# Kernel optimization log

Measured on AMD Instinct MI355X. Metric: run time of the kernel, lower is better.

## Reference

```python
import jax, jax.numpy as jnp
import numpy as np

N, E = 8192, 65536
IN_C, OUT_C, EF = 64, 16, 8
L1, L2 = 48, 32  # in - floor((in-out)/3), in - floor(2*(in-out)/3)


def setup_inputs() -> dict:
    key = jax.random.key(0)
    ks = jax.random.split(key, 10)
    rn = lambda k, shape, s: jax.random.normal(k, shape, dtype=jnp.float32) * s
    return {
        "x": jax.random.normal(ks[0], (N, IN_C), dtype=jnp.float32),
        "edge_index": jax.random.randint(ks[1], (2, E), 0, N, dtype=jnp.int32),
        "edge_attr": jax.random.normal(ks[2], (E, EF), dtype=jnp.float32),
        "nn1_w": rn(ks[3], (EF, IN_C * L1), 0.05),
        "nn1_b": jnp.zeros((IN_C * L1,), jnp.float32),
        "root1": rn(ks[4], (IN_C, L1), 0.1),
        "bias1": jnp.zeros((L1,), jnp.float32),
        "nn2_w": rn(ks[5], (EF, L1 * L2), 0.05),
        "nn2_b": jnp.zeros((L1 * L2,), jnp.float32),
        "root2": rn(ks[6], (L1, L2), 0.1),
        "bias2": jnp.zeros((L2,), jnp.float32),
        "mu_w": rn(ks[7], (L2, OUT_C), 0.1),
        "mu_b": jnp.zeros((OUT_C,), jnp.float32),
        "ls_w": rn(ks[8], (L2, OUT_C), 0.1),
        "ls_b": jnp.zeros((OUT_C,), jnp.float32),
    }


def _nnconv(x, src, dst, edge_attr, nn_w, nn_b, root, bias, c_in, c_out):
    # edge MLP -> per-edge weight matrices [E, c_in, c_out]
    w = (edge_attr @ nn_w + nn_b).reshape(-1, c_in, c_out)
    msg = jnp.einsum('ei,eio->eo', x[src], w)  # gather + per-edge matvec
    agg = jax.ops.segment_sum(msg, dst, num_segments=x.shape[0])  # sum aggregation
    return agg + x @ root + bias  # root transform + bias


def _gcn(x, src, dst, w, b):
    n = x.shape[0]
    # degree over target nodes, including self-loop (edge_weight = 1)
    deg = jax.ops.segment_sum(jnp.ones_like(src, jnp.float32), dst, num_segments=n) + 1.0
    dinv = jax.lax.rsqrt(deg)
    h = x @ w
    norm = dinv[src] * dinv[dst]  # [E]
    agg = jax.ops.segment_sum(h[src] * norm[:, None], dst, num_segments=n)
    return agg + h * (1.0 / deg)[:, None] + b  # self-loop contribution: deg_i^{-1}


def reference(x, edge_index, edge_attr, nn1_w, nn1_b, root1, bias1,
              nn2_w, nn2_b, root2, bias2, mu_w, mu_b, ls_w, ls_b):
    src, dst = edge_index[0], edge_index[1]
    h = jax.nn.relu(_nnconv(x, src, dst, edge_attr, nn1_w, nn1_b, root1, bias1, IN_C, L1))
    h = jax.nn.relu(_nnconv(h, src, dst, edge_attr, nn2_w, nn2_b, root2, bias2, L1, L2))
    return (_gcn(h, src, dst, mu_w, mu_b), _gcn(h, src, dst, ls_w, ls_b))
```

## Files before the change

kernel.cpp:

```cpp
#include <hip/hip_runtime.h>

#define NN 8192
#define EE 65536
#define MAXDEG 32
#define ZS1 652
#define ZS2 492
#define U1_OFF 5216
#define U2_OFF 3936


__global__ __launch_bounds__(256) void k_zero(int* __restrict__ cnt,
                                              int* __restrict__ ssrcb,
                                              float* __restrict__ seab) {
    int n = blockIdx.x * 256 + threadIdx.x;
    cnt[n] = 0;
    ssrcb[n * MAXDEG] = 0;
    float4* p = (float4*)(seab + (size_t)n * MAXDEG * 8);
    p[0] = make_float4(0.f, 0.f, 0.f, 0.f);
    p[1] = make_float4(0.f, 0.f, 0.f, 0.f);
}

__global__ __launch_bounds__(256) void k_bucket(const int* __restrict__ ei,
                                                const float* __restrict__ ea,
                                                int* __restrict__ cnt,
                                                int* __restrict__ ssrcb,
                                                float* __restrict__ seab) {
    int e = blockIdx.x * 256 + threadIdx.x;
    if (e >= EE) return;
    int s = ei[e], d = ei[EE + e];
    int pos = atomicAdd(&cnt[d], 1);
    if (pos < MAXDEG) {
        int slot = d * MAXDEG + pos;
        ssrcb[slot] = s;
        const float4* a = (const float4*)(ea + (size_t)e * 8);
        float4* bp = (float4*)(seab + (size_t)slot * 8);
        bp[0] = a[0];
        bp[1] = a[1];
    }
}

__global__ __launch_bounds__(256) void k_L1(const int* __restrict__ cnt,
                                            const int* __restrict__ ssrcb,
                                            const float* __restrict__ seab,
                                            const float* __restrict__ x,
                                            const float* __restrict__ nn1_w,
                                            const float* __restrict__ nn1_b,
                                            const float* __restrict__ root1,
                                            const float* __restrict__ bias1,
                                            float* __restrict__ h1) {
    __shared__ __align__(16) float smem[U1_OFF + 3072];
    float* Zt = smem;
    float* U  = smem + U1_OFF;
    const int n0 = blockIdx.x * 8;
    {
        const int wv = threadIdx.x >> 6;
        const int i = threadIdx.x & 63;
        const int nnA = wv * 2, nnB = nnA + 1;
        const int rsA = (n0 + nnA) * MAXDEG;
        const int rsB = (n0 + nnB) * MAXDEG;
        int dA = cnt[n0 + nnA]; if (dA > MAXDEG) dA = MAXDEG;
        int dB = cnt[n0 + nnB]; if (dB > MAXDEG) dB = MAXDEG;
        const int eA = rsA + dA, eB = rsB + dB;
        int jA = rsA, jB = rsB;
        float aA[8] = {0, 0, 0, 0, 0, 0, 0, 0}, sA = 0.f;
        float aB[8] = {0, 0, 0, 0, 0, 0, 0, 0}, sB = 0.f;
        while (jA < eA || jB < eB) {
            int cjA[8], cjB[8];
#pragma unroll
            for (int p = 0; p < 8; p++) {
                int ja = jA + p; cjA[p] = (ja < eA) ? ja : rsA;
                int jb = jB + p; cjB[p] = (jb < eB) ? jb : rsB;
            }
            int sjA[8], sjB[8];
#pragma unroll
            for (int p = 0; p < 8; p++) { sjA[p] = ssrcb[cjA[p]]; sjB[p] = ssrcb[cjB[p]]; }
            float xvA[8], xvB[8];
#pragma unroll
            for (int p = 0; p < 8; p++) {
                xvA[p] = x[(size_t)sjA[p] * 64 + i];
                xvB[p] = x[(size_t)sjB[p] * 64 + i];
            }
#pragma unroll
            for (int p = 0; p < 8; p++) {
                {
                    const float4* q4 = (const float4*)(seab + (size_t)cjA[p] * 8);
                    float4 e0 = q4[0], e1 = q4[1];
                    float xx = (jA + p < eA) ? xvA[p] : 0.f;
                    aA[0] += e0.x * xx; aA[1] += e0.y * xx; aA[2] += e0.z * xx; aA[3] += e0.w * xx;
                    aA[4] += e1.x * xx; aA[5] += e1.y * xx; aA[6] += e1.z * xx; aA[7] += e1.w * xx;
                    sA += xx;
                }
                {
                    const float4* q4 = (const float4*)(seab + (size_t)cjB[p] * 8);
                    float4 e0 = q4[0], e1 = q4[1];
                    float xx = (jB + p < eB) ? xvB[p] : 0.f;
                    aB[0] += e0.x * xx; aB[1] += e0.y * xx; aB[2] += e0.z * xx; aB[3] += e0.w * xx;
                    aB[4] += e1.x * xx; aB[5] += e1.y * xx; aB[6] += e1.z * xx; aB[7] += e1.w * xx;
                    sB += xx;
                }
            }
            jA += 8; jB += 8;
        }
        float* zrA = Zt + nnA * ZS1;
        float* zrB = Zt + nnB * ZS1;
#pragma unroll
        for (int f = 0; f < 8; f++) { zrA[f * 64 + i] = aA[f]; zrB[f * 64 + i] = aB[f]; }
        zrA[512 + i] = sA; zrB[512 + i] = sB;
        zrA[576 + i] = x[(size_t)(n0 + nnA) * 64 + i];
        zrB[576 + i] = x[(size_t)(n0 + nnB) * 64 + i];
    }
    const int o  = threadIdx.x & 15;
    const int q  = (threadIdx.x >> 4) & 1;
    const int ks = threadIdx.x >> 5;
    float acc[4][3];
#pragma unroll
    for (int m = 0; m < 4; m++)
#pragma unroll
        for (int cc = 0; cc < 3; cc++) acc[m][cc] = 0.f;
    for (int c = 0; c < 10; ++c) {
        __syncthreads();
        const float* src = (c < 8) ? nn1_w + c * 3072 : (c == 8 ? nn1_b : root1);
#pragma unroll
        for (int i2 = 0; i2 < 3; i2++) {
            int g = threadIdx.x + i2 * 256;
            *(float4*)&U[g * 4] = *(const float4*)&src[g * 4];
        }
        __syncthreads();
        const int kl0 = ks * 8;
        const int kg0 = c * 64 + kl0;
#pragma unroll
        for (int kk = 0; kk < 8; kk += 4) {
            const int kl = kl0 + kk, kg = kg0 + kk;
            float zc[4][4];
#pragma unroll
            for (int m = 0; m < 4; m++) {
                float4 z = *(const float4*)&Zt[(q * 4 + m) * ZS1 + kg];
                zc[m][0] = z.x; zc[m][1] = z.y; zc[m][2] = z.z; zc[m][3] = z.w;
            }
#pragma unroll
            for (int dk = 0; dk < 4; dk++) {
                float w0 = U[(kl + dk) * 48 + o];
                float w1 = U[(kl + dk) * 48 + o + 16];
                float w2 = U[(kl + dk) * 48 + o + 32];
#pragma unroll
                for (int m = 0; m < 4; m++) {
                    acc[m][0] += zc[m][dk] * w0;
                    acc[m][1] += zc[m][dk] * w1;
                    acc[m][2] += zc[m][dk] * w2;
                }
            }
        }
    }
    __syncthreads();
#pragma unroll
    for (int m = 0; m < 4; m++) {
        U[(ks * 8 + q * 4 + m) * 48 + o]      = acc[m][0];
        U[(ks * 8 + q * 4 + m) * 48 + o + 16] = acc[m][1];
        U[(ks * 8 + q * 4 + m) * 48 + o + 32] = acc[m][2];
    }
    __syncthreads();
    for (int r = threadIdx.x; r < 8 * 48; r += 256) {
        int nn = r / 48, oc = r - nn * 48;
        float v = bias1[oc];
#pragma unroll
        for (int k = 0; k < 8; k++) v += U[(k * 8 + nn) * 48 + oc];
        h1[(size_t)(n0 + nn) * 48 + oc] = v > 0.f ? v : 0.f;
    }
}

__global__ __launch_bounds__(256) void k_L2(const int* __restrict__ cnt,
                                            const int* __restrict__ ssrcb,
                                            const float* __restrict__ seab,
                                            const float* __restrict__ h1,
                                            const float* __restrict__ nn2_w,
                                            const float* __restrict__ nn2_b,
                                            const float* __restrict__ root2,
                                            const float* __restrict__ bias2,
                                            const float* __restrict__ mu_w,
                                            const float* __restrict__ mu_b,
                                            const float* __restrict__ ls_w,
                                            const float* __restrict__ ls_b,
                                            float* __restrict__ hmu,
                                            float* __restrict__ hls,
                                            float* __restrict__ dinv,
                                            float* __restrict__ out) {
    __shared__ __align__(16) float smem[U2_OFF + 3072];
    float* Zt = smem;
    float* U  = smem + U2_OFF;
    const int n0 = blockIdx.x * 8;
    {
        const int wv = threadIdx.x >> 6;
        const int i = threadIdx.x & 63;
        if (i < 48) {
            const int nnA = wv * 2, nnB = nnA + 1;
            const int rsA = (n0 + nnA) * MAXDEG;
            const int rsB = (n0 + nnB) * MAXDEG;
            int dA = cnt[n0 + nnA]; if (dA > MAXDEG) dA = MAXDEG;
            int dB = cnt[n0 + nnB]; if (dB > MAXDEG) dB = MAXDEG;
            const int eA = rsA + dA, eB = rsB + dB;
            int jA = rsA, jB = rsB;
            float aA[8] = {0, 0, 0, 0, 0, 0, 0, 0}, sA = 0.f;
            float aB[8] = {0, 0, 0, 0, 0, 0, 0, 0}, sB = 0.f;
            while (jA < eA || jB < eB) {
                int cjA[8], cjB[8];
#pragma unroll
                for (int p = 0; p < 8; p++) {
                    int ja = jA + p; cjA[p] = (ja < eA) ? ja : rsA;
                    int jb = jB + p; cjB[p] = (jb < eB) ? jb : rsB;
                }
                int sjA[8], sjB[8];
#pragma unroll
                for (int p = 0; p < 8; p++) { sjA[p] = ssrcb[cjA[p]]; sjB[p] = ssrcb[cjB[p]]; }
                float hvA[8], hvB[8];
#pragma unroll
                for (int p = 0; p < 8; p++) {
                    hvA[p] = h1[(size_t)sjA[p] * 48 + i];
                    hvB[p] = h1[(size_t)sjB[p] * 48 + i];
                }
#pragma unroll
                for (int p = 0; p < 8; p++) {
                    {
                        const float4* q4 = (const float4*)(seab + (size_t)cjA[p] * 8);
                        float4 e0 = q4[0], e1 = q4[1];
                        float xx = (jA + p < eA) ? hvA[p] : 0.f;
                        aA[0] += e0.x * xx; aA[1] += e0.y * xx; aA[2] += e0.z * xx; aA[3] += e0.w * xx;
                        aA[4] += e1.x * xx; aA[5] += e1.y * xx; aA[6] += e1.z * xx; aA[7] += e1.w * xx;
                        sA += xx;
                    }
                    {
                        const float4* q4 = (const float4*)(seab + (size_t)cjB[p] * 8);
                        float4 e0 = q4[0], e1 = q4[1];
                        float xx = (jB + p < eB) ? hvB[p] : 0.f;
                        aB[0] += e0.x * xx; aB[1] += e0.y * xx; aB[2] += e0.z * xx; aB[3] += e0.w * xx;
                        aB[4] += e1.x * xx; aB[5] += e1.y * xx; aB[6] += e1.z * xx; aB[7] += e1.w * xx;
                        sB += xx;
                    }
                }
                jA += 8; jB += 8;
            }
            float* zrA = Zt + nnA * ZS2;
            float* zrB = Zt + nnB * ZS2;
#pragma unroll
            for (int f = 0; f < 8; f++) { zrA[f * 48 + i] = aA[f]; zrB[f * 48 + i] = aB[f]; }
            zrA[384 + i] = sA; zrB[384 + i] = sB;
            zrA[432 + i] = h1[(size_t)(n0 + nnA) * 48 + i];
            zrB[432 + i] = h1[(size_t)(n0 + nnB) * 48 + i];
        }
    }
    const int o  = threadIdx.x & 15;
    const int q  = (threadIdx.x >> 4) & 1;
    const int ks = threadIdx.x >> 5;
    float acc[4][2];
#pragma unroll
    for (int m = 0; m < 4; m++) { acc[m][0] = 0.f; acc[m][1] = 0.f; }
    for (int c = 0; c < 5; ++c) {
        __syncthreads();
#pragma unroll
        for (int i2 = 0; i2 < 3; i2++) {
            int g = threadIdx.x + i2 * 256;
            const float* s4;
            if (c < 4)        s4 = nn2_w + c * 3072 + g * 4;
            else if (g < 384) s4 = nn2_b + g * 4;
            else              s4 = root2 + (g - 384) * 4;
            *(float4*)&U[g * 4] = *(const float4*)s4;
        }
        __syncthreads();
        const int kl0 = ks * 12;
        const int kg0 = c * 96 + kl0;
#pragma unroll
        for (int kk = 0; kk < 12; kk += 4) {
            const int kl = kl0 + kk, kg = kg0 + kk;
            float zc[4][4];
#pragma unroll
            for (int m = 0; m < 4; m++) {
                float4 z = *(const float4*)&Zt[(q * 4 + m) * ZS2 + kg];
                zc[m][0] = z.x; zc[m][1] = z.y; zc[m][2] = z.z; zc[m][3] = z.w;
            }
#pragma unroll
            for (int dk = 0; dk < 4; dk++) {
                float w0 = U[(kl + dk) * 32 + o];
                float w1 = U[(kl + dk) * 32 + o + 16];
#pragma unroll
                for (int m = 0; m < 4; m++) {
                    acc[m][0] += zc[m][dk] * w0;
                    acc[m][1] += zc[m][dk] * w1;
                }
            }
        }
    }
    __syncthreads();
#pragma unroll
    for (int m = 0; m < 4; m++) {
        U[(ks * 8 + q * 4 + m) * 32 + o]      = acc[m][0];
        U[(ks * 8 + q * 4 + m) * 32 + o + 16] = acc[m][1];
    }
    __syncthreads();
    {
        int nn = threadIdx.x >> 5, oc = threadIdx.x & 31;
        float v = bias2[oc];
#pragma unroll
        for (int k = 0; k < 8; k++) v += U[(k * 8 + nn) * 32 + oc];
        U[2048 + nn * 33 + oc] = v > 0.f ? v : 0.f;
    }
    __syncthreads();
    if (threadIdx.x < 128) {
        const int oc = threadIdx.x & 15;
        const int nn = threadIdx.x >> 4;
        const int gn = n0 + nn;
        float am = 0.f, al = 0.f;
#pragma unroll
        for (int i = 0; i < 32; i++) {
            float hv = U[2048 + nn * 33 + i];
            am += hv * mu_w[i * 16 + oc];
            al += hv * ls_w[i * 16 + oc];
        }
        float d = (float)cnt[gn] + 1.0f;
        float di = rsqrtf(d);
        if (oc == 0) dinv[gn] = di;
        hmu[(size_t)gn * 16 + oc] = am;
        hls[(size_t)gn * 16 + oc] = al;
        out[(size_t)gn * 16 + oc] = am / d + mu_b[oc];
        out[(size_t)NN * 16 + (size_t)gn * 16 + oc] = al / d + ls_b[oc];
    }
}

__global__ __launch_bounds__(256) void k_gcn(const int* __restrict__ cnt,
                                             const int* __restrict__ ssrcb,
                                             const float* __restrict__ hmu,
                                             const float* __restrict__ hls,
                                             const float* __restrict__ dinv,
                                             float* __restrict__ out) {
    const int wave = threadIdx.x >> 6;
    const int lane = threadIdx.x & 63;
    const int o = lane & 15, p = lane >> 4;
    const int d = blockIdx.x * 4 + wave;
    int deg = cnt[d]; if (deg > MAXDEG) deg = MAXDEG;
    const int rs = d * MAXDEG, re = rs + deg;
    float am = 0.f, al = 0.f;
    for (int j = rs + p; j < re; j += 4) {
        int s = ssrcb[j];
        float ds_ = dinv[s];
        am += hmu[(size_t)s * 16 + o] * ds_;
        al += hls[(size_t)s * 16 + o] * ds_;
    }
    am += __shfl_xor(am, 16); al += __shfl_xor(al, 16);
    am += __shfl_xor(am, 32); al += __shfl_xor(al, 32);
    if (p == 0) {
        float dd = dinv[d];
        out[(size_t)d * 16 + o] += am * dd;
        out[(size_t)NN * 16 + (size_t)d * 16 + o] += al * dd;
    }
}

extern "C" void kernel_launch(void* const* d_in, const int* in_sizes, int n_in,
                              void* d_out, int out_size, void* d_ws, size_t ws_size,
                              hipStream_t stream) {
    const float* x     = (const float*)d_in[0];
    const int*   ei    = (const int*)d_in[1];
    const float* ea    = (const float*)d_in[2];
    const float* nn1_w = (const float*)d_in[3];
    const float* nn1_b = (const float*)d_in[4];
    const float* root1 = (const float*)d_in[5];
    const float* bias1 = (const float*)d_in[6];
    const float* nn2_w = (const float*)d_in[7];
    const float* nn2_b = (const float*)d_in[8];
    const float* root2 = (const float*)d_in[9];
    const float* bias2 = (const float*)d_in[10];
    const float* mu_w  = (const float*)d_in[11];
    const float* mu_b  = (const float*)d_in[12];
    const float* ls_w  = (const float*)d_in[13];
    const float* ls_b  = (const float*)d_in[14];
    float* out = (float*)d_out;

    float* W    = (float*)d_ws;
    float* seab = W;
    float* h1   = seab + NN * MAXDEG * 8;
    float* hmu  = h1 + 393216;
    float* hls  = hmu + 131072;
    float* dinv = hls + 131072;
    int* cnt    = (int*)(dinv + 8192);
    int* ssrcb  = cnt + 8192;

    k_zero<<<dim3(NN / 256), dim3(256), 0, stream>>>(cnt, ssrcb, seab);
    k_bucket<<<dim3(EE / 256), dim3(256), 0, stream>>>(ei, ea, cnt, ssrcb, seab);
    k_L1<<<dim3(NN / 8), dim3(256), 0, stream>>>(cnt, ssrcb, seab, x,
                                                 nn1_w, nn1_b, root1, bias1, h1);
    k_L2<<<dim3(NN / 8), dim3(256), 0, stream>>>(cnt, ssrcb, seab, h1,
                                                 nn2_w, nn2_b, root2, bias2,
                                                 mu_w, mu_b, ls_w, ls_b,
                                                 hmu, hls, dinv, out);
    k_gcn<<<dim3(NN / 4), dim3(256), 0, stream>>>(cnt, ssrcb,
                                                  hmu, hls, dinv, out);
}
```

Measured before the change: 149.5 us.

## Pre-transpose edge-MLP weights, swizzle LDS tiles, prefetch weight chunks, unroll GCN gather

The bucket kernel now also writes transposed copies of the concatenated edge-MLP weight, bias and root matrices into workspace. This lets the L1/L2 GEMM loops read float4 weight vectors along K from an XOR-swizzled LDS layout, which cuts LDS read instructions and bank conflicts. The next weight chunk is loaded from global memory into registers while the current chunk is being used, and self-feature loads are issued early. The GCN gather processes two edges per iteration to raise memory-level parallelism, at the cost of extra registers and a small transpose on every call.

```diff
diff --git a/kernel.cpp b/kernel.cpp
--- a/kernel.cpp
+++ b/kernel.cpp
@@ -5,6 +5,8 @@
 #define MAXDEG 32
 #define ZS1 652
 #define ZS2 492
+#define WS1 68
+#define WS2 100
 #define U1_OFF 5216
 #define U2_OFF 3936
 
@@ -22,10 +24,32 @@
 
 __global__ __launch_bounds__(256) void k_bucket(const int* __restrict__ ei,
                                                 const float* __restrict__ ea,
+                                                const float* __restrict__ nn1_w,
+                                                const float* __restrict__ nn1_b,
+                                                const float* __restrict__ root1,
+                                                const float* __restrict__ nn2_w,
+                                                const float* __restrict__ nn2_b,
+                                                const float* __restrict__ root2,
                                                 int* __restrict__ cnt,
                                                 int* __restrict__ ssrcb,
-                                                float* __restrict__ seab) {
+                                                float* __restrict__ seab,
+                                                float* __restrict__ WtT1,
+                                                float* __restrict__ WtT2) {
     int e = blockIdx.x * 256 + threadIdx.x;
+    if (e < 48 * 640) {
+        int col = e / 640, k = e - col * 640;
+        float v = (k < 512) ? nn1_w[k * 48 + col]
+                : (k < 576) ? nn1_b[(k - 512) * 48 + col]
+                            : root1[(k - 576) * 48 + col];
+        WtT1[e] = v;
+    } else if (e < 48 * 640 + 32 * 480) {
+        int r = e - 48 * 640;
+        int col = r / 480, k = r - col * 480;
+        float v = (k < 384) ? nn2_w[k * 32 + col]
+                : (k < 432) ? nn2_b[(k - 384) * 32 + col]
+                            : root2[(k - 432) * 32 + col];
+        WtT2[r] = v;
+    }
     if (e >= EE) return;
     int s = ei[e], d = ei[EE + e];
     int pos = atomicAdd(&cnt[d], 1);
@@ -43,12 +67,10 @@
                                             const int* __restrict__ ssrcb,
                                             const float* __restrict__ seab,
                                             const float* __restrict__ x,
-                                            const float* __restrict__ nn1_w,
-                                            const float* __restrict__ nn1_b,
-                                            const float* __restrict__ root1,
+                                            const float* __restrict__ WtT1,
                                             const float* __restrict__ bias1,
                                             float* __restrict__ h1) {
-    __shared__ __align__(16) float smem[U1_OFF + 3072];
+    __shared__ __align__(16) float smem[U1_OFF + 48 * WS1];
     float* Zt = smem;
     float* U  = smem + U1_OFF;
     const int n0 = blockIdx.x * 8;
@@ -58,6 +80,8 @@
         const int nnA = wv * 2, nnB = nnA + 1;
         const int rsA = (n0 + nnA) * MAXDEG;
         const int rsB = (n0 + nnB) * MAXDEG;
+        float xselfA = x[(size_t)(n0 + nnA) * 64 + i];
+        float xselfB = x[(size_t)(n0 + nnB) * 64 + i];
         int dA = cnt[n0 + nnA]; if (dA > MAXDEG) dA = MAXDEG;
         int dB = cnt[n0 + nnB]; if (dB > MAXDEG) dB = MAXDEG;
         const int eA = rsA + dA, eB = rsB + dB;
@@ -106,48 +130,57 @@
 #pragma unroll
         for (int f = 0; f < 8; f++) { zrA[f * 64 + i] = aA[f]; zrB[f * 64 + i] = aB[f]; }
         zrA[512 + i] = sA; zrB[512 + i] = sB;
-        zrA[576 + i] = x[(size_t)(n0 + nnA) * 64 + i];
-        zrB[576 + i] = x[(size_t)(n0 + nnB) * 64 + i];
+        zrA[576 + i] = xselfA;
+        zrB[576 + i] = xselfB;
     }
     const int o  = threadIdx.x & 15;
     const int q  = (threadIdx.x >> 4) & 1;
     const int ks = threadIdx.x >> 5;
+    const int xsw = (o & 7) << 2;
+    const int g0 = threadIdx.x, g1 = threadIdx.x + 256, g2 = threadIdx.x + 512;
+    const int c0_ = g0 >> 4, k0_ = (g0 & 15) << 2;
+    const int c1_ = g1 >> 4, k1_ = (g1 & 15) << 2;
+    const int c2_ = g2 >> 4, k2_ = (g2 & 15) << 2;
+    const int sa0 = c0_ * WS1 + (k0_ ^ ((c0_ & 7) << 2));
+    const int sa1 = c1_ * WS1 + (k1_ ^ ((c1_ & 7) << 2));
+    const int sa2 = c2_ * WS1 + (k2_ ^ ((c2_ & 7) << 2));
+    const float* gp0 = WtT1 + c0_ * 640 + k0_;
+    const float* gp1 = WtT1 + c1_ * 640 + k1_;
+    const float* gp2 = WtT1 + c2_ * 640 + k2_;
     float acc[4][3];
 #pragma unroll
     for (int m = 0; m < 4; m++)
 #pragma unroll
         for (int cc = 0; cc < 3; cc++) acc[m][cc] = 0.f;
+    float4 r0 = *(const float4*)gp0;
+    float4 r1 = *(const float4*)gp1;
+    float4 r2 = *(const float4*)gp2;
     for (int c = 0; c < 10; ++c) {
         __syncthreads();
-        const float* src = (c < 8) ? nn1_w + c * 3072 : (c == 8 ? nn1_b : root1);
-#pragma unroll
-        for (int i2 = 0; i2 < 3; i2++) {
-            int g = threadIdx.x + i2 * 256;
-            *(float4*)&U[g * 4] = *(const float4*)&src[g * 4];
-        }
+        *(float4*)&U[sa0] = r0;
+        *(float4*)&U[sa1] = r1;
+        *(float4*)&U[sa2] = r2;
         __syncthreads();
-        const int kl0 = ks * 8;
-        const int kg0 = c * 64 + kl0;
+        if (c < 9) {
+            r0 = *(const float4*)(gp0 + (c + 1) * 64);
+            r1 = *(const float4*)(gp1 + (c + 1) * 64);
+            r2 = *(const float4*)(gp2 + (c + 1) * 64);
+        }
 #pragma unroll
         for (int kk = 0; kk < 8; kk += 4) {
-            const int kl = kl0 + kk, kg = kg0 + kk;
-            float zc[4][4];
+            const int kl = ks * 8 + kk;
+            const int kx = kl ^ xsw;
+            const int kg = c * 64 + kl;
+            float4 w0 = *(const float4*)&U[o * WS1 + kx];
+            float4 w1 = *(const float4*)&U[(o + 16) * WS1 + kx];
+            float4 w2 = *(const float4*)&U[(o + 32) * WS1 + kx];
 #pragma unroll
             for (int m = 0; m < 4; m++) {
                 float4 z = *(const float4*)&Zt[(q * 4 + m) * ZS1 + kg];
-                zc[m][0] = z.x; zc[m][1] = z.y; zc[m][2] = z.z; zc[m][3] = z.w;
-            }
-#pragma unroll
-            for (int dk = 0; dk < 4; dk++) {
-                float w0 = U[(kl + dk) * 48 + o];
-                float w1 = U[(kl + dk) * 48 + o + 16];
-                float w2 = U[(kl + dk) * 48 + o + 32];
-#pragma unroll
-                for (int m = 0; m < 4; m++) {
-                    acc[m][0] += zc[m][dk] * w0;
-                    acc[m][1] += zc[m][dk] * w1;
-                    acc[m][2] += zc[m][dk] * w2;
-                }
+                acc[m][0] += z.x * w0.x; acc[m][1] += z.x * w1.x; acc[m][2] += z.x * w2.x;
+                acc[m][0] += z.y * w0.y; acc[m][1] += z.y * w1.y; acc[m][2] += z.y * w2.y;
+                acc[m][0] += z.z * w0.z; acc[m][1] += z.z * w1.z; acc[m][2] += z.z * w2.z;
+                acc[m][0] += z.w * w0.w; acc[m][1] += z.w * w1.w; acc[m][2] += z.w * w2.w;
             }
         }
     }
@@ -172,9 +205,7 @@
                                             const int* __restrict__ ssrcb,
                                             const float* __restrict__ seab,
                                             const float* __restrict__ h1,
-                                            const float* __restrict__ nn2_w,
-                                            const float* __restrict__ nn2_b,
-                                            const float* __restrict__ root2,
+                                            const float* __restrict__ WtT2,
                                             const float* __restrict__ bias2,
                                             const float* __restrict__ mu_w,
                                             const float* __restrict__ mu_b,
@@ -184,7 +215,7 @@
                                             float* __restrict__ hls,
                                             float* __restrict__ dinv,
                                             float* __restrict__ out) {
-    __shared__ __align__(16) float smem[U2_OFF + 3072];
+    __shared__ __align__(16) float smem[U2_OFF + 32 * WS2];
     float* Zt = smem;
     float* U  = smem + U2_OFF;
     const int n0 = blockIdx.x * 8;
@@ -195,6 +226,8 @@
             const int nnA = wv * 2, nnB = nnA + 1;
             const int rsA = (n0 + nnA) * MAXDEG;
             const int rsB = (n0 + nnB) * MAXDEG;
+            float hselfA = h1[(size_t)(n0 + nnA) * 48 + i];
+            float hselfB = h1[(size_t)(n0 + nnB) * 48 + i];
             int dA = cnt[n0 + nnA]; if (dA > MAXDEG) dA = MAXDEG;
             int dB = cnt[n0 + nnB]; if (dB > MAXDEG) dB = MAXDEG;
             const int eA = rsA + dA, eB = rsB + dB;
@@ -243,48 +276,55 @@
 #pragma unroll
             for (int f = 0; f < 8; f++) { zrA[f * 48 + i] = aA[f]; zrB[f * 48 + i] = aB[f]; }
             zrA[384 + i] = sA; zrB[384 + i] = sB;
-            zrA[432 + i] = h1[(size_t)(n0 + nnA) * 48 + i];
-            zrB[432 + i] = h1[(size_t)(n0 + nnB) * 48 + i];
+            zrA[432 + i] = hselfA;
+            zrB[432 + i] = hselfB;
         }
     }
     const int o  = threadIdx.x & 15;
     const int q  = (threadIdx.x >> 4) & 1;
     const int ks = threadIdx.x >> 5;
+    const int xsw = (o & 7) << 2;
+    const int g0 = threadIdx.x, g1 = threadIdx.x + 256, g2 = threadIdx.x + 512;
+    const int c0_ = g0 / 24, k0_ = (g0 - c0_ * 24) << 2;
+    const int c1_ = g1 / 24, k1_ = (g1 - c1_ * 24) << 2;
+    const int c2_ = g2 / 24, k2_ = (g2 - c2_ * 24) << 2;
+    const int sa0 = c0_ * WS2 + (k0_ ^ ((c0_ & 7) << 2));
+    const int sa1 = c1_ * WS2 + (k1_ ^ ((c1_ & 7) << 2));
+    const int sa2 = c2_ * WS2 + (k2_ ^ ((c2_ & 7) << 2));
+    const float* gp0 = WtT2 + c0_ * 480 + k0_;
+    const float* gp1 = WtT2 + c1_ * 480 + k1_;
+    const float* gp2 = WtT2 + c2_ * 480 + k2_;
     float acc[4][2];
 #pragma unroll
     for (int m = 0; m < 4; m++) { acc[m][0] = 0.f; acc[m][1] = 0.f; }
+    float4 r0 = *(const float4*)gp0;
+    float4 r1 = *(const float4*)gp1;
+    float4 r2 = *(const float4*)gp2;
     for (int c = 0; c < 5; ++c) {
         __syncthreads();
-#pragma unroll
-        for (int i2 = 0; i2 < 3; i2++) {
-            int g = threadIdx.x + i2 * 256;
-            const float* s4;
-            if (c < 4)        s4 = nn2_w + c * 3072 + g * 4;
-            else if (g < 384) s4 = nn2_b + g * 4;
-            else              s4 = root2 + (g - 384) * 4;
-            *(float4*)&U[g * 4] = *(const float4*)s4;
-        }
+        *(float4*)&U[sa0] = r0;
+        *(float4*)&U[sa1] = r1;
+        *(float4*)&U[sa2] = r2;
         __syncthreads();
-        const int kl0 = ks * 12;
-        const int kg0 = c * 96 + kl0;
+        if (c < 4) {
+            r0 = *(const float4*)(gp0 + (c + 1) * 96);
+            r1 = *(const float4*)(gp1 + (c + 1) * 96);
+            r2 = *(const float4*)(gp2 + (c + 1) * 96);
+        }
 #pragma unroll
         for (int kk = 0; kk < 12; kk += 4) {
-            const int kl = kl0 + kk, kg = kg0 + kk;
-            float zc[4][4];
+            const int kl = ks * 12 + kk;
+            const int kx = kl ^ xsw;
+            const int kg = c * 96 + kl;
+            float4 w0 = *(const float4*)&U[o * WS2 + kx];
+            float4 w1 = *(const float4*)&U[(o + 16) * WS2 + kx];
 #pragma unroll
             for (int m = 0; m < 4; m++) {
                 float4 z = *(const float4*)&Zt[(q * 4 + m) * ZS2 + kg];
-                zc[m][0] = z.x; zc[m][1] = z.y; zc[m][2] = z.z; zc[m][3] = z.w;
-            }
-#pragma unroll
-            for (int dk = 0; dk < 4; dk++) {
-                float w0 = U[(kl + dk) * 32 + o];
-                float w1 = U[(kl + dk) * 32 + o + 16];
-#pragma unroll
-                for (int m = 0; m < 4; m++) {
-                    acc[m][0] += zc[m][dk] * w0;
-                    acc[m][1] += zc[m][dk] * w1;
-                }
+                acc[m][0] += z.x * w0.x; acc[m][1] += z.x * w1.x;
+                acc[m][0] += z.y * w0.y; acc[m][1] += z.y * w1.y;
+                acc[m][0] += z.z * w0.z; acc[m][1] += z.z * w1.z;
+                acc[m][0] += z.w * w0.w; acc[m][1] += z.w * w1.w;
             }
         }
     }
@@ -337,11 +377,15 @@
     int deg = cnt[d]; if (deg > MAXDEG) deg = MAXDEG;
     const int rs = d * MAXDEG, re = rs + deg;
     float am = 0.f, al = 0.f;
-    for (int j = rs + p; j < re; j += 4) {
-        int s = ssrcb[j];
-        float ds_ = dinv[s];
-        am += hmu[(size_t)s * 16 + o] * ds_;
-        al += hls[(size_t)s * 16 + o] * ds_;
+    for (int j = rs + p; j < re; j += 8) {
+        int jb = j + 4;
+        int sa = ssrcb[j];
+        int sb = ssrcb[jb < re ? jb : rs];
+        float da_ = dinv[sa], db_ = dinv[sb];
+        float ma = hmu[(size_t)sa * 16 + o], la = hls[(size_t)sa * 16 + o];
+        float mb = hmu[(size_t)sb * 16 + o], lb = hls[(size_t)sb * 16 + o];
+        am += ma * da_; al += la * da_;
+        if (jb < re) { am += mb * db_; al += lb * db_; }
     }
     am += __shfl_xor(am, 16); al += __shfl_xor(al, 16);
     am += __shfl_xor(am, 32); al += __shfl_xor(al, 32);
@@ -372,21 +416,26 @@
     const float* ls_b  = (const float*)d_in[14];
     float* out = (float*)d_out;
 
-    float* W    = (float*)d_ws;
-    float* seab = W;
-    float* h1   = seab + NN * MAXDEG * 8;
-    float* hmu  = h1 + 393216;
-    float* hls  = hmu + 131072;
-    float* dinv = hls + 131072;
-    int* cnt    = (int*)(dinv + 8192);
-    int* ssrcb  = cnt + 8192;
+    float* W     = (float*)d_ws;
+    float* WtT1  = W;
+    float* WtT2  = WtT1 + 30720;
+    float* seab  = WtT2 + 15360;
+    float* h1    = seab + NN * MAXDEG * 8;
+    float* hmu   = h1 + 393216;
+    float* hls   = hmu + 131072;
+    float* dinv  = hls + 131072;
+    int* cnt     = (int*)(dinv + 8192);
+    int* ssrcb   = cnt + 8192;
 
     k_zero<<<dim3(NN / 256), dim3(256), 0, stream>>>(cnt, ssrcb, seab);
-    k_bucket<<<dim3(EE / 256), dim3(256), 0, stream>>>(ei, ea, cnt, ssrcb, seab);
+    k_bucket<<<dim3(EE / 256), dim3(256), 0, stream>>>(ei, ea,
+                                                       nn1_w, nn1_b, root1,
+                                                       nn2_w, nn2_b, root2,
+                                                       cnt, ssrcb, seab, WtT1, WtT2);
     k_L1<<<dim3(NN / 8), dim3(256), 0, stream>>>(cnt, ssrcb, seab, x,
-                                                 nn1_w, nn1_b, root1, bias1, h1);
+                                                 WtT1, bias1, h1);
     k_L2<<<dim3(NN / 8), dim3(256), 0, stream>>>(cnt, ssrcb, seab, h1,
-                                                 nn2_w, nn2_b, root2, bias2,
+                                                 WtT2, bias2,
                                                  mu_w, mu_b, ls_w, ls_b,
                                                  hmu, hls, dinv, out);
     k_gcn<<<dim3(NN / 4), dim3(256), 0, stream>>>(cnt, ssrcb,
```

Result: faster. 145.5 us (-2.7%).
